# Kernel optimization log

Measured on AMD Instinct MI355X. Metric: run time of the kernel, lower is better.

## Reference

```python
import jax, jax.numpy as jnp
import numpy as np

B, S, N, DEG, KC = 4, 12, 8192, 16, 3
SEQ = S - KC + 1  # 10
H, LAYER, HID, MLP_H = 4, 3, 3, 64
NEG = -1e9


def setup_inputs() -> dict:
    key = jax.random.key(0)
    ks = jax.random.split(key, 40)
    f = lambda i, shp, sc=0.2: jax.random.normal(ks[i], shp, jnp.float32) * sc
    # deterministic unique edge list: DEG distinct neighbors per source node
    src = np.repeat(np.arange(N), DEG)
    dst = (src + 1 + np.tile(np.arange(DEG), N) * 37) % N
    edges = jnp.asarray(np.stack([src, dst]).astype(np.int32))
    return dict(
        occ=jax.random.normal(ks[0], (B, S, N), jnp.float32),
        prc_l=jax.random.uniform(ks[1], (B, N), jnp.float32),
        edges=edges,
        values=jnp.ones((N * DEG,), jnp.float32),
        conv_w=f(2, (1, 1, KC, 2)), conv_b=f(3, (1,)),
        gat_W=f(4, (H, SEQ, SEQ)), gat_a=f(5, (H, 2 * SEQ)),
        gat_lin_w=f(6, (1, H)), gat_lin_b=f(7, (1,)),
        gcn_w=f(8, (SEQ, SEQ)), gcn_b=f(9, (SEQ,)),
        Wih0=f(10, (4 * HID, LAYER)), Whh0=f(11, (4 * HID, HID)), bih0=f(12, (4 * HID,)), bhh0=f(13, (4 * HID,)),
        Wih1=f(14, (4 * HID, HID)), Whh1=f(15, (4 * HID, HID)), bih1=f(16, (4 * HID,)), bhh1=f(17, (4 * HID,)),
        Qw=f(18, (SEQ, SEQ)), Kw=f(19, (SEQ, SEQ)), Vw=f(20, (SEQ, SEQ)),
        m1w1=f(21, (MLP_H, SEQ)), m1b1=f(22, (MLP_H,)),
        m1w2=f(23, (MLP_H // 2, MLP_H)), m1b2=f(24, (MLP_H // 2,)),
        m1w3=f(25, (1, MLP_H // 2)), m1b3=f(26, (1,)),
        m2w1=f(27, (8 * (LAYER + 1), LAYER + 1)), m2b1=f(28, (8 * (LAYER + 1),)),
        m2w2=f(29, (4 * (LAYER + 1), 8 * (LAYER + 1))), m2b2=f(30, (4 * (LAYER + 1),)),
        m2w3=f(31, (1, 4 * (LAYER + 1))), m2b3=f(32, (1,)),
    )


def _lstm_layer(x, Wih, Whh, bih, bhh):
    # x: [T, Bn, in] time-major; PyTorch gate order i,f,g,o
    Bn, hdim = x.shape[1], Whh.shape[1]
    def step(carry, xt):
        h, c = carry
        g = xt @ Wih.T + h @ Whh.T + bih + bhh
        i, fg, gg, o = jnp.split(g, 4, axis=1)
        c = jax.nn.sigmoid(fg) * c + jax.nn.sigmoid(i) * jnp.tanh(gg)
        h = jax.nn.sigmoid(o) * jnp.tanh(c)
        return (h, c), h
    init = (jnp.zeros((Bn, hdim), x.dtype), jnp.zeros((Bn, hdim), x.dtype))
    _, hs = jax.lax.scan(step, init, x)
    return hs  # [T, Bn, hdim]


def _gat(x2, src, dst, values, mask, gat_W, gat_a, lin_w, lin_b):
    # x2: [b*n, seq]; only first N rows are gathered (faithful to the original)
    h = jnp.einsum('ns,hso->hno', x2, gat_W)                 # [H, b*n, seq]
    eh = jnp.concatenate([h[:, src, :], h[:, dst, :]], 2)    # [H, E, 2*seq]
    atts = jax.nn.leaky_relu(jnp.einsum('hed,hd->he', eh, gat_a), 0.2)  # [H, E]
    mt = atts.T @ lin_w.T + lin_b                            # [E, 1]
    new_vals = values * mt[:, 0]
    n = mask.shape[0]
    dense = jnp.zeros((n, n), x2.dtype).at[src, dst].add(new_vals)
    return jax.nn.softmax(dense + mask, axis=0)              # softmax over dim 0, as nn.Softmax(dim=0)


def reference(occ, prc_l, edges, values, conv_w, conv_b, gat_W, gat_a, gat_lin_w, gat_lin_b, gcn_w, gcn_b, Wih0, Whh0, bih0, bhh0, Wih1, Whh1, bih1, bhh1, Qw, Kw, Vw, m1w1, m1b1, m1w2, m1b2, m1w3, m1b3, m2w1, m2b1, m2w2, m2b2, m2w3, m2b3):
    b, s, n = occ.shape
    seq = s - conv_w.shape[2] + 1
    occ_t = jnp.transpose(occ, (0, 2, 1))                    # [b, n, s]
    prc = jnp.broadcast_to(prc_l[:, :, None], (b, n, s))
    fea = jnp.stack([occ_t, prc], axis=3).reshape(b * n, s, 2)[:, None]  # [bn,1,s,2]
    fea = jax.lax.conv_general_dilated(fea, conv_w, (1, 1), 'VALID',
                                       dimension_numbers=('NCHW', 'OIHW', 'NCHW'))
    fea = (fea + conv_b[None, :, None, None]).reshape(b, n, seq)
    src, dst = edges[0], edges[1]
    mask = jnp.full((n, n), NEG, occ.dtype).at[src, dst].set(0.0)
    lrelu = lambda z: jax.nn.leaky_relu(z, 0.01)
    gcn = lambda z: lrelu(z @ gcn_w.T + gcn_b)
    A1 = _gat(fea.reshape(b * n, seq), src, dst, values, mask, gat_W, gat_a, gat_lin_w, gat_lin_b)
    c1 = gcn(jnp.einsum('nm,bms->bns', A1, fea))
    A2 = _gat(c1.reshape(b * n, seq), src, dst, values, mask, gat_W, gat_a, gat_lin_w, gat_lin_b)
    c2 = gcn(jnp.einsum('nm,bms->bns', A2, c1))
    xt = jnp.stack([fea, c1, c2], axis=3).reshape(b * n, seq, 3)
    xT = jnp.transpose(xt, (1, 0, 2))                        # time-major [seq, bn, 3]
    h0 = _lstm_layer(xT, Wih0, Whh0, bih0, bhh0)
    h1 = _lstm_layer(h0, Wih1, Whh1, bih1, bhh1)
    x_long = jnp.transpose(h1, (1, 0, 2))                    # [bn, seq, 3]
    y_long = x_long[:, -1, 0]                                # [bn]
    xl = jnp.transpose(x_long, (0, 2, 1))                    # [bn, 3, seq]
    Q = xl @ Qw.T
    K = xl @ Kw.T
    V = xl @ Vw.T
    alpha = jax.nn.softmax(jnp.einsum('bis,bjs->bij', Q, K) / jnp.float32(V.shape[1]), axis=2)
    att = jnp.einsum('bij,bjs->bis', alpha, V)               # [bn, 3, seq]
    h = jax.nn.relu(att @ m1w1.T + m1b1)
    h = jax.nn.relu(h @ m1w2.T + m1b2)
    att_out = (h @ m1w3.T + m1b3)[:, :, 0]                   # [bn, 3]
    temp = jnp.concatenate([y_long[:, None], att_out], axis=1)  # [bn, 4]
    h = jax.nn.relu(temp @ m2w1.T + m2b1)
    h = jax.nn.relu(h @ m2w2.T + m2b2)
    y = (h @ m2w3.T + m2b3)[:, 0]
    return y.reshape(b, n)
```

## Files before the change

### kernel.cpp

```cpp
#include <hip/hip_runtime.h>

#define NN    8192
#define BB    4
#define SS    12
#define SEQL  10
#define SEQP  16
#define KCC   3
#define DEGN  16
#define EE    (NN*DEGN)
#define HHH   4
#define HIDN  3
#define BN    (BB*NN)

__device__ __forceinline__ float fexp(float x)  { return __expf(x); }
__device__ __forceinline__ float fsig(float x)  { return __fdividef(1.0f, 1.0f + __expf(-x)); }

__global__ __launch_bounds__(256) void k_fea_node(const float* __restrict__ occ,
                                                  const float* __restrict__ prc,
                                                  const float* __restrict__ convw,
                                                  const float* __restrict__ convb,
                                                  const float* __restrict__ gatW,
                                                  const float* __restrict__ gata,
                                                  float* __restrict__ fea,
                                                  float* __restrict__ p1p2) {
    int t = blockIdx.x * blockDim.x + threadIdx.x;
    if (t >= BN) return;
    int b = t >> 13, nn = t & (NN - 1);
    float o[SS];
    const float* op = occ + (size_t)b * SS * NN + nn;
#pragma unroll
    for (int s = 0; s < SS; s++) o[s] = op[(size_t)s * NN];
    float w0[KCC], w1s = 0.f;
#pragma unroll
    for (int k = 0; k < KCC; k++) { w0[k] = convw[k * 2]; w1s += convw[k * 2 + 1]; }
    float base = prc[t] * w1s + convb[0];
    float fv[SEQL];
#pragma unroll
    for (int tt = 0; tt < SEQL; tt++) {
        float acc = base;
#pragma unroll
        for (int k = 0; k < KCC; k++) acc += o[tt + k] * w0[k];
        fv[tt] = acc;
    }
    float* f = fea + (size_t)t * SEQP;
    *(float4*)(f)     = make_float4(fv[0], fv[1], fv[2], fv[3]);
    *(float4*)(f + 4) = make_float4(fv[4], fv[5], fv[6], fv[7]);
    *(float2*)(f + 8) = make_float2(fv[8], fv[9]);
    if (t < NN) {
#pragma unroll
        for (int hh = 0; hh < HHH; hh++) {
            float p1 = 0.f, p2 = 0.f;
#pragma unroll
            for (int oo = 0; oo < SEQL; oo++) {
                float hv = 0.f;
#pragma unroll
                for (int s = 0; s < SEQL; s++) hv += fv[s] * gatW[hh * (SEQL * SEQL) + s * SEQL + oo];
                p1 += hv * gata[hh * (2 * SEQL) + oo];
                p2 += hv * gata[hh * (2 * SEQL) + SEQL + oo];
            }
            p1p2[t * 8 + hh]     = p1;
            p1p2[t * 8 + 4 + hh] = p2;
        }
    }
}

__global__ __launch_bounds__(256) void k_colmt(const float* __restrict__ values,
                                               const float* __restrict__ p1p2,
                                               const float* __restrict__ linw,
                                               const float* __restrict__ linb,
                                               float* __restrict__ mt,
                                               float2* __restrict__ colms) {
    int u = blockIdx.x * blockDim.x + threadIdx.x;
    int q = u & 3, j = u >> 2;
    float p2l[HHH], lw[HHH];
#pragma unroll
    for (int hh = 0; hh < HHH; hh++) { p2l[hh] = p1p2[j * 8 + 4 + hh]; lw[hh] = linw[hh]; }
    float lb = linb[0];
    float v[4];
#pragma unroll
    for (int dd = 0; dd < 4; dd++) {
        int d = q * 4 + dd;
        int s = (j - 1 - d * 37) & (NN - 1);
        int e = s * DEGN + d;
        float4 p1v = *(const float4*)(p1p2 + s * 8);
        float a0 = p1v.x + p2l[0]; a0 = a0 > 0.f ? a0 : 0.2f * a0;
        float a1 = p1v.y + p2l[1]; a1 = a1 > 0.f ? a1 : 0.2f * a1;
        float a2 = p1v.z + p2l[2]; a2 = a2 > 0.f ? a2 : 0.2f * a2;
        float a3 = p1v.w + p2l[3]; a3 = a3 > 0.f ? a3 : 0.2f * a3;
        float acc = lb + a0*lw[0] + a1*lw[1] + a2*lw[2] + a3*lw[3];
        float m_ = acc * values[e];
        v[dd] = m_;
        mt[e] = m_;
    }
    float m = fmaxf(fmaxf(v[0], v[1]), fmaxf(v[2], v[3]));
    m = fmaxf(m, __shfl_xor(m, 1));
    m = fmaxf(m, __shfl_xor(m, 2));
    float sum = 0.f;
#pragma unroll
    for (int dd = 0; dd < 4; dd++) sum += fexp(v[dd] - m);
    sum += __shfl_xor(sum, 1);
    sum += __shfl_xor(sum, 2);
    if (q == 0) colms[j] = make_float2(m, __fdividef(1.0f, sum));
}

template <int DOP>
__global__ __launch_bounds__(256) void k_agg(const int* __restrict__ edges,
                                             const float* __restrict__ mt,
                                             const float2* __restrict__ colms,
                                             const float* __restrict__ xin,
                                             const float* __restrict__ gcnw,
                                             const float* __restrict__ gcnb,
                                             const float* __restrict__ gatW,
                                             const float* __restrict__ gata,
                                             float* __restrict__ xout,
                                             float* __restrict__ p1p2) {
    int u = blockIdx.x * blockDim.x + threadIdx.x;
    int q = u & 7, t = u >> 3;
    int b = t >> 13, i = t & (NN - 1);
    int e0 = i * DEGN + q * 2;
    int2   dn2 = *(const int2*)(edges + EE + e0);
    float2 mt2 = *(const float2*)(mt + e0);
    int dns[2] = {dn2.x, dn2.y};
    float mts[2] = {mt2.x, mt2.y};
    float acc[SEQL];
#pragma unroll
    for (int s = 0; s < SEQL; s++) acc[s] = 0.f;
#pragma unroll
    for (int dd = 0; dd < 2; dd++) {
        int dn = dns[dd];
        float2 ms = colms[dn];
        float w = fexp(mts[dd] - ms.x) * ms.y;
        const float* xr = xin + ((size_t)b * NN + dn) * SEQP;
        float4 v0 = *(const float4*)(xr);
        float4 v1 = *(const float4*)(xr + 4);
        float2 v2 = *(const float2*)(xr + 8);
        acc[0] += w*v0.x; acc[1] += w*v0.y; acc[2] += w*v0.z; acc[3] += w*v0.w;
        acc[4] += w*v1.x; acc[5] += w*v1.y; acc[6] += w*v1.z; acc[7] += w*v1.w;
        acc[8] += w*v2.x; acc[9] += w*v2.y;
    }
#pragma unroll
    for (int s = 0; s < SEQL; s++) acc[s] += __shfl_xor(acc[s], 1);
#pragma unroll
    for (int s = 0; s < SEQL; s++) acc[s] += __shfl_xor(acc[s], 2);
#pragma unroll
    for (int s = 0; s < SEQL; s++) acc[s] += __shfl_xor(acc[s], 4);

    float co[SEQL];
#pragma unroll
    for (int o = 0; o < SEQL; o++) {
        float a = gcnb[o];
#pragma unroll
        for (int s = 0; s < SEQL; s++) a += acc[s] * gcnw[o * SEQL + s];
        co[o] = a > 0.f ? a : 0.01f * a;
    }
    if (q == 0) {
        float* xo = xout + (size_t)t * SEQP;
        *(float4*)(xo)     = make_float4(co[0], co[1], co[2], co[3]);
        *(float4*)(xo + 4) = make_float4(co[4], co[5], co[6], co[7]);
        *(float2*)(xo + 8) = make_float2(co[8], co[9]);
    }
    if (DOP && t < NN && q < 4) {
        float hv[SEQL];
#pragma unroll
        for (int oo = 0; oo < SEQL; oo++) hv[oo] = 0.f;
#pragma unroll
        for (int s = 0; s < SEQL; s++) {
            const float2* wr = (const float2*)(gatW + q * (SEQL*SEQL) + s * SEQL);
#pragma unroll
            for (int p = 0; p < 5; p++) {
                float2 wv = wr[p];
                hv[2*p]   += co[s] * wv.x;
                hv[2*p+1] += co[s] * wv.y;
            }
        }
        const float2* ga1 = (const float2*)(gata + q * (2*SEQL));
        const float2* ga2 = (const float2*)(gata + q * (2*SEQL) + SEQL);
        float p1 = 0.f, p2 = 0.f;
#pragma unroll
        for (int p = 0; p < 5; p++) {
            float2 a1 = ga1[p], a2 = ga2[p];
            p1 += hv[2*p] * a1.x + hv[2*p+1] * a1.y;
            p2 += hv[2*p] * a2.x + hv[2*p+1] * a2.y;
        }
        p1p2[t * 8 + q]     = p1;
        p1p2[t * 8 + 4 + q] = p2;
    }
}

__global__ __launch_bounds__(256) void k_lstm_att(
    const float* __restrict__ fea, const float* __restrict__ c1g, const float* __restrict__ c2g,
    const float* __restrict__ Wih0, const float* __restrict__ Whh0,
    const float* __restrict__ bih0, const float* __restrict__ bhh0,
    const float* __restrict__ Wih1, const float* __restrict__ Whh1,
    const float* __restrict__ bih1, const float* __restrict__ bhh1,
    const float* __restrict__ Qw, const float* __restrict__ Kw, const float* __restrict__ Vw,
    float* __restrict__ attrow) {

    int u = blockIdx.x * blockDim.x + threadIdx.x;
    int e = u & 1;
    int t = u >> 1;

    float fr[SEQL], c1r[SEQL], c2r[SEQL];
    {
        const float* a = fea + (size_t)t * SEQP;
        const float* b = c1g + (size_t)t * SEQP;
        const float* c = c2g + (size_t)t * SEQP;
        float4 a0 = *(const float4*)a, a1 = *(const float4*)(a+4); float2 a2 = *(const float2*)(a+8);
        float4 b0 = *(const float4*)b, b1 = *(const float4*)(b+4); float2 b2 = *(const float2*)(b+8);
        float4 d0 = *(const float4*)c, d1 = *(const float4*)(c+4); float2 d2 = *(const float2*)(c+8);
        fr[0]=a0.x; fr[1]=a0.y; fr[2]=a0.z; fr[3]=a0.w; fr[4]=a1.x; fr[5]=a1.y; fr[6]=a1.z; fr[7]=a1.w; fr[8]=a2.x; fr[9]=a2.y;
        c1r[0]=b0.x; c1r[1]=b0.y; c1r[2]=b0.z; c1r[3]=b0.w; c1r[4]=b1.x; c1r[5]=b1.y; c1r[6]=b1.z; c1r[7]=b1.w; c1r[8]=b2.x; c1r[9]=b2.y;
        c2r[0]=d0.x; c2r[1]=d0.y; c2r[2]=d0.z; c2r[3]=d0.w; c2r[4]=d1.x; c2r[5]=d1.y; c2r[6]=d1.z; c2r[7]=d1.w; c2r[8]=d2.x; c2r[9]=d2.y;
    }

    int r0 = e * 6;
    float W0[6][6], B0[6], W1[6][6], B1[6];
#pragma unroll
    for (int k = 0; k < 6; k++) {
        int r = r0 + k;
        W0[k][0]=Wih0[r*3]; W0[k][1]=Wih0[r*3+1]; W0[k][2]=Wih0[r*3+2];
        W0[k][3]=Whh0[r*3]; W0[k][4]=Whh0[r*3+1]; W0[k][5]=Whh0[r*3+2];
        B0[k]=bih0[r]+bhh0[r];
        W1[k][0]=Wih1[r*3]; W1[k][1]=Wih1[r*3+1]; W1[k][2]=Wih1[r*3+2];
        W1[k][3]=Whh1[r*3]; W1[k][4]=Whh1[r*3+1]; W1[k][5]=Whh1[r*3+2];
        B1[k]=bih1[r]+bhh1[r];
    }
    float two_e = e ? 2.f : 1.f;
    float neg_e = e ? -1.f : 0.f;

    float c0[3]={0,0,0}, c1s[3]={0,0,0}, h0[3]={0,0,0}, h1[3]={0,0,0};
    float hist[SEQL][HIDN];
#pragma unroll
    for (int st = 0; st < SEQL; st++) {
        float tt[6], pp[6];
        {
            float x0 = fr[st], x1 = c1r[st], x2 = c2r[st];
#pragma unroll
            for (int k = 0; k < 6; k++) {
                float g = B0[k] + x0*W0[k][0] + x1*W0[k][1] + x2*W0[k][2]
                                + h0[0]*W0[k][3] + h0[1]*W0[k][4] + h0[2]*W0[k][5];
                if (k < 3) { float uu = fsig(two_e * g); tt[k] = two_e * uu + neg_e; }
                else       { tt[k] = fsig(g); }
            }
#pragma unroll
            for (int k = 0; k < 6; k++) pp[k] = __shfl_xor(tt[k], 1);
#pragma unroll
            for (int j = 0; j < 3; j++) {
                float si = e ? pp[j]   : tt[j];
                float sf = e ? pp[3+j] : tt[3+j];
                float tg = e ? tt[j]   : pp[j];
                float so = e ? tt[3+j] : pp[3+j];
                float cn = sf * c0[j] + si * tg;
                c0[j] = cn;
                h0[j] = so * (2.f * fsig(2.f * cn) - 1.f);
            }
        }
        {
#pragma unroll
            for (int k = 0; k < 6; k++) {
                float g = B1[k] + h0[0]*W1[k][0] + h0[1]*W1[k][1] + h0[2]*W1[k][2]
                                + h1[0]*W1[k][3] + h1[1]*W1[k][4] + h1[2]*W1[k][5];
                if (k < 3) { float uu = fsig(two_e * g); tt[k] = two_e * uu + neg_e; }
                else       { tt[k] = fsig(g); }
            }
#pragma unroll
            for (int k = 0; k < 6; k++) pp[k] = __shfl_xor(tt[k], 1);
#pragma unroll
            for (int j = 0; j < 3; j++) {
                float si = e ? pp[j]   : tt[j];
                float sf = e ? pp[3+j] : tt[3+j];
                float tg = e ? tt[j]   : pp[j];
                float so = e ? tt[3+j] : pp[3+j];
                float cn = sf * c1s[j] + si * tg;
                c1s[j] = cn;
                h1[j] = so * (2.f * fsig(2.f * cn) - 1.f);
            }
        }
#pragma unroll
        for (int j = 0; j < 3; j++) hist[st][j] = h1[j];
    }

    float V[3][5];
    float sc[3][3];
#pragma unroll
    for (int a = 0; a < 3; a++)
#pragma unroll
        for (int j = 0; j < 3; j++) sc[a][j] = 0.f;
#pragma unroll
    for (int p = 0; p < 5; p++) {
        int o = 2 * p + e;
        float wq[SEQL], wk[SEQL], wv[SEQL];
        const float2* q2 = (const float2*)(Qw + o * SEQL);
        const float2* k2 = (const float2*)(Kw + o * SEQL);
        const float2* v2 = (const float2*)(Vw + o * SEQL);
#pragma unroll
        for (int z = 0; z < 5; z++) {
            float2 a = q2[z], b = k2[z], c = v2[z];
            wq[2*z] = a.x; wq[2*z+1] = a.y;
            wk[2*z] = b.x; wk[2*z+1] = b.y;
            wv[2*z] = c.x; wv[2*z+1] = c.y;
        }
        float qj[3], kj[3];
#pragma unroll
        for (int j = 0; j < 3; j++) {
            float qv = 0.f, kv = 0.f, vv = 0.f;
#pragma unroll
            for (int s = 0; s < SEQL; s++) {
                float xv = hist[s][j];
                qv += xv * wq[s]; kv += xv * wk[s]; vv += xv * wv[s];
            }
            qj[j] = qv; kj[j] = kv; V[j][p] = vv;
        }
#pragma unroll
        for (int a = 0; a < 3; a++)
#pragma unroll
            for (int j = 0; j < 3; j++) sc[a][j] += qj[a] * kj[j];
    }
#pragma unroll
    for (int a = 0; a < 3; a++)
#pragma unroll
        for (int j = 0; j < 3; j++) sc[a][j] += __shfl_xor(sc[a][j], 1);

    float* ar = attrow + (size_t)t * 32;
#pragma unroll
    for (int a = 0; a < 3; a++) {
        float s0 = sc[a][0] * (1.f/3.f), s1 = sc[a][1] * (1.f/3.f), s2 = sc[a][2] * (1.f/3.f);
        float m = fmaxf(s0, fmaxf(s1, s2));
        float e0 = fexp(s0-m), e1 = fexp(s1-m), e2 = fexp(s2-m);
        float inv = __fdividef(1.0f, e0 + e1 + e2);
#pragma unroll
        for (int p = 0; p < 5; p++)
            ar[a * SEQL + 2*p + e] = (e0*V[0][p] + e1*V[1][p] + e2*V[2][p]) * inv;
    }
    if (e == 0) ar[30] = hist[SEQL-1][0];
}

__global__ __launch_bounds__(256, 2) void k_head(
    const float* __restrict__ attrow,
    const float* __restrict__ m1w1, const float* __restrict__ m1b1,
    const float* __restrict__ m1w2, const float* __restrict__ m1b2,
    const float* __restrict__ m1w3, const float* __restrict__ m1b3,
    const float* __restrict__ m2w1, const float* __restrict__ m2b1,
    const float* __restrict__ m2w2, const float* __restrict__ m2b2,
    const float* __restrict__ m2w3, const float* __restrict__ m2b3,
    float* __restrict__ out) {

    __shared__ float lw[3717];
    int tid = threadIdx.x;
    for (int z = tid; z < 1024; z += 256) {
        int qq = z >> 8, kk = (z >> 4) & 15, s = z & 15;
        if (s < 12) lw[qq*200 + kk*12 + s] = (s < 10) ? m1w1[(qq*16+kk)*10 + s] : 0.f;
    }
    for (int z = tid; z < 2048; z += 256) {
        int qq = z >> 9, rem = z & 511, r = rem >> 4, kk = rem & 15;
        lw[800 + qq*520 + r*16 + kk] = m1w2[r*64 + qq*16 + kk];
    }
    for (int z = tid; z < 64;  z += 256) lw[2880 + z] = m1b1[z];
    for (int z = tid; z < 32;  z += 256) { lw[2944 + z] = m1b2[z]; lw[2976 + z] = m1w3[z]; }
    for (int z = tid; z < 128; z += 256) lw[3012 + z] = m2w1[z];
    for (int z = tid; z < 32;  z += 256) lw[3140 + z] = m2b1[z];
    for (int z = tid; z < 512; z += 256) lw[3172 + z] = m2w2[z];
    for (int z = tid; z < 16;  z += 256) { lw[3684 + z] = m2b2[z]; lw[3700 + z] = m2w3[z]; }
    if (tid == 0) { lw[3008] = m1b3[0]; lw[3716] = m2b3[0]; }
    __syncthreads();

    int u = blockIdx.x * blockDim.x + tid;
    int q = u & 3;
    int t = u >> 2;

    const float* w1b = lw + q * 200;
    float hb0[16], hb1[16], hb2a[16];
    float ylong;
    {
        float row[32];
        const float4* arp = (const float4*)(attrow + (size_t)t * 32);
#pragma unroll
        for (int p = 0; p < 8; p++) {
            float4 z = arp[p];
            row[4*p] = z.x; row[4*p+1] = z.y; row[4*p+2] = z.z; row[4*p+3] = z.w;
        }
        ylong = row[30];
#pragma unroll 4
        for (int kk = 0; kk < 16; kk++) {
            float4 wa = *(const float4*)(w1b + kk*12);
            float4 wb = *(const float4*)(w1b + kk*12 + 4);
            float4 wc = *(const float4*)(w1b + kk*12 + 8);
            float bk = lw[2880 + q*16 + kk];
            float a0 = bk
                + row[0]*wa.x + row[1]*wa.y + row[2]*wa.z + row[3]*wa.w
                + row[4]*wb.x + row[5]*wb.y + row[6]*wb.z + row[7]*wb.w
                + row[8]*wc.x + row[9]*wc.y;
            float a1 = bk
                + row[10]*wa.x + row[11]*wa.y + row[12]*wa.z + row[13]*wa.w
                + row[14]*wb.x + row[15]*wb.y + row[16]*wb.z + row[17]*wb.w
                + row[18]*wc.x + row[19]*wc.y;
            float a2 = bk
                + row[20]*wa.x + row[21]*wa.y + row[22]*wa.z + row[23]*wa.w
                + row[24]*wb.x + row[25]*wb.y + row[26]*wb.z + row[27]*wb.w
                + row[28]*wc.x + row[29]*wc.y;
            hb0[kk] = a0 > 0.f ? a0 : 0.f;
            hb1[kk] = a1 > 0.f ? a1 : 0.f;
            hb2a[kk] = a2 > 0.f ? a2 : 0.f;
        }
    }

    const float* w2b = lw + 800 + q * 520;
    float ao0 = lw[3008], ao1 = ao0, ao2 = ao0;
#pragma unroll 4
    for (int r = 0; r < 32; r++) {
        const float4* wr = (const float4*)(w2b + r * 16);
        float4 w0 = wr[0], w1 = wr[1], w2 = wr[2], w3 = wr[3];
        float p0 = hb0[0]*w0.x + hb0[1]*w0.y + hb0[2]*w0.z + hb0[3]*w0.w
                 + hb0[4]*w1.x + hb0[5]*w1.y + hb0[6]*w1.z + hb0[7]*w1.w
                 + hb0[8]*w2.x + hb0[9]*w2.y + hb0[10]*w2.z + hb0[11]*w2.w
                 + hb0[12]*w3.x + hb0[13]*w3.y + hb0[14]*w3.z + hb0[15]*w3.w;
        float p1 = hb1[0]*w0.x + hb1[1]*w0.y + hb1[2]*w0.z + hb1[3]*w0.w
                 + hb1[4]*w1.x + hb1[5]*w1.y + hb1[6]*w1.z + hb1[7]*w1.w
                 + hb1[8]*w2.x + hb1[9]*w2.y + hb1[10]*w2.z + hb1[11]*w2.w
                 + hb1[12]*w3.x + hb1[13]*w3.y + hb1[14]*w3.z + hb1[15]*w3.w;
        float p2 = hb2a[0]*w0.x + hb2a[1]*w0.y + hb2a[2]*w0.z + hb2a[3]*w0.w
                 + hb2a[4]*w1.x + hb2a[5]*w1.y + hb2a[6]*w1.z + hb2a[7]*w1.w
                 + hb2a[8]*w2.x + hb2a[9]*w2.y + hb2a[10]*w2.z + hb2a[11]*w2.w
                 + hb2a[12]*w3.x + hb2a[13]*w3.y + hb2a[14]*w3.z + hb2a[15]*w3.w;
        p0 += __shfl_xor(p0, 1); p0 += __shfl_xor(p0, 2);
        p1 += __shfl_xor(p1, 1); p1 += __shfl_xor(p1, 2);
        p2 += __shfl_xor(p2, 1); p2 += __shfl_xor(p2, 2);
        float bb = lw[2944 + r], ww = lw[2976 + r];
        float t0 = p0 + bb; t0 = t0 > 0.f ? t0 : 0.f;
        float t1 = p1 + bb; t1 = t1 > 0.f ? t1 : 0.f;
        float t2 = p2 + bb; t2 = t2 > 0.f ? t2 : 0.f;
        ao0 += t0 * ww; ao1 += t1 * ww; ao2 += t2 * ww;
    }

    float hb2[32];
#pragma unroll 8
    for (int k = 0; k < 32; k++) {
        float4 wv = *(const float4*)(lw + 3012 + k*4);
        float a = lw[3140 + k] + ylong*wv.x + ao0*wv.y + ao1*wv.z + ao2*wv.w;
        hb2[k] = a > 0.f ? a : 0.f;
    }
    float y = lw[3716];
#pragma unroll 4
    for (int r = 0; r < 16; r++) {
        float a = lw[3684 + r];
        const float4* wr = (const float4*)(lw + 3172 + r*32);
#pragma unroll
        for (int c = 0; c < 8; c++) {
            float4 wv = wr[c];
            a += hb2[4*c]*wv.x + hb2[4*c+1]*wv.y + hb2[4*c+2]*wv.z + hb2[4*c+3]*wv.w;
        }
        float h = a > 0.f ? a : 0.f;
        y += h * lw[3700 + r];
    }
    if (q == 0) out[t] = y;
}

extern "C" void kernel_launch(void* const* d_in, const int* in_sizes, int n_in,
                              void* d_out, int out_size, void* d_ws, size_t ws_size,
                              hipStream_t stream) {
    const float* occ    = (const float*)d_in[0];
    const float* prc    = (const float*)d_in[1];
    const int*   edges  = (const int*)  d_in[2];
    const float* values = (const float*)d_in[3];
    const float* convw  = (const float*)d_in[4];
    const float* convb  = (const float*)d_in[5];
    const float* gatW   = (const float*)d_in[6];
    const float* gata   = (const float*)d_in[7];
    const float* linw   = (const float*)d_in[8];
    const float* linb   = (const float*)d_in[9];
    const float* gcnw   = (const float*)d_in[10];
    const float* gcnb   = (const float*)d_in[11];
    const float* Wih0   = (const float*)d_in[12];
    const float* Whh0   = (const float*)d_in[13];
    const float* bih0   = (const float*)d_in[14];
    const float* bhh0   = (const float*)d_in[15];
    const float* Wih1   = (const float*)d_in[16];
    const float* Whh1   = (const float*)d_in[17];
    const float* bih1   = (const float*)d_in[18];
    const float* bhh1   = (const float*)d_in[19];
    const float* Qw     = (const float*)d_in[20];
    const float* Kw     = (const float*)d_in[21];
    const float* Vw     = (const float*)d_in[22];
    const float* m1w1   = (const float*)d_in[23];
    const float* m1b1   = (const float*)d_in[24];
    const float* m1w2   = (const float*)d_in[25];
    const float* m1b2   = (const float*)d_in[26];
    const float* m1w3   = (const float*)d_in[27];
    const float* m1b3   = (const float*)d_in[28];
    const float* m2w1   = (const float*)d_in[29];
    const float* m2b1   = (const float*)d_in[30];
    const float* m2w2   = (const float*)d_in[31];
    const float* m2b2   = (const float*)d_in[32];
    const float* m2w3   = (const float*)d_in[33];
    const float* m2b3   = (const float*)d_in[34];
    float* out = (float*)d_out;

    char* ws = (char*)d_ws;
    float*  fea    = (float*) (ws);
    float*  c1     = (float*) (ws + 2097152);
    float*  c2     = (float*) (ws + 4194304);
    float*  p1p2   = (float*) (ws + 6291456);
    float*  mt     = (float*) (ws + 6553600);
    float2* colms  = (float2*)(ws + 7077888);
    float*  attrow = (float*) (ws + 7143424);

    k_fea_node<<<128, 256, 0, stream>>>(occ, prc, convw, convb, gatW, gata, fea, p1p2);

    k_colmt<<<128, 256, 0, stream>>>(values, p1p2, linw, linb, mt, colms);
    k_agg<1><<<1024, 256, 0, stream>>>(edges, mt, colms, fea, gcnw, gcnb,
                                       gatW, gata, c1, p1p2);

    k_colmt<<<128, 256, 0, stream>>>(values, p1p2, linw, linb, mt, colms);
    k_agg<0><<<1024, 256, 0, stream>>>(edges, mt, colms, c1, gcnw, gcnb,
                                       gatW, gata, c2, p1p2);

    k_lstm_att<<<256, 256, 0, stream>>>(fea, c1, c2,
        Wih0, Whh0, bih0, bhh0, Wih1, Whh1, bih1, bhh1, Qw, Kw, Vw, attrow);

    k_head<<<512, 256, 0, stream>>>(attrow,
        m1w1, m1b1, m1w2, m1b2, m1w3, m1b3,
        m2w1, m2b1, m2w2, m2b2, m2w3, m2b3, out);
}
```

Before: 78.22 us.

## Fuse LSTM-attention kernel with MLP head kernel

Merges the LSTM/attention kernel and the MLP head kernel into one launch. Attention outputs are exchanged via warp shuffles and kept in registers instead of being written to and reread from a global attrow buffer. Each node now uses four threads, so the LSTM/attention computation is duplicated across thread pairs, and the combined kernel carries higher register pressure.

```diff
diff --git a/kernel.cpp b/kernel.cpp
--- a/kernel.cpp
+++ b/kernel.cpp
@@ -187,18 +187,44 @@
     }
 }
 
-__global__ __launch_bounds__(256) void k_lstm_att(
+__global__ __launch_bounds__(256, 2) void k_lstm_head(
     const float* __restrict__ fea, const float* __restrict__ c1g, const float* __restrict__ c2g,
     const float* __restrict__ Wih0, const float* __restrict__ Whh0,
     const float* __restrict__ bih0, const float* __restrict__ bhh0,
     const float* __restrict__ Wih1, const float* __restrict__ Whh1,
     const float* __restrict__ bih1, const float* __restrict__ bhh1,
     const float* __restrict__ Qw, const float* __restrict__ Kw, const float* __restrict__ Vw,
-    float* __restrict__ attrow) {
-
-    int u = blockIdx.x * blockDim.x + threadIdx.x;
-    int e = u & 1;
-    int t = u >> 1;
+    const float* __restrict__ m1w1, const float* __restrict__ m1b1,
+    const float* __restrict__ m1w2, const float* __restrict__ m1b2,
+    const float* __restrict__ m1w3, const float* __restrict__ m1b3,
+    const float* __restrict__ m2w1, const float* __restrict__ m2b1,
+    const float* __restrict__ m2w2, const float* __restrict__ m2b2,
+    const float* __restrict__ m2w3, const float* __restrict__ m2b3,
+    float* __restrict__ out) {
+
+    __shared__ float lw[3717];
+    int tid = threadIdx.x;
+    for (int z = tid; z < 1024; z += 256) {
+        int qq = z >> 8, kk = (z >> 4) & 15, s = z & 15;
+        if (s < 12) lw[qq*200 + kk*12 + s] = (s < 10) ? m1w1[(qq*16+kk)*10 + s] : 0.f;
+    }
+    for (int z = tid; z < 2048; z += 256) {
+        int qq = z >> 9, rem = z & 511, r = rem >> 4, kk = rem & 15;
+        lw[800 + qq*520 + r*16 + kk] = m1w2[r*64 + qq*16 + kk];
+    }
+    for (int z = tid; z < 64;  z += 256) lw[2880 + z] = m1b1[z];
+    for (int z = tid; z < 32;  z += 256) { lw[2944 + z] = m1b2[z]; lw[2976 + z] = m1w3[z]; }
+    for (int z = tid; z < 128; z += 256) lw[3012 + z] = m2w1[z];
+    for (int z = tid; z < 32;  z += 256) lw[3140 + z] = m2b1[z];
+    for (int z = tid; z < 512; z += 256) lw[3172 + z] = m2w2[z];
+    for (int z = tid; z < 16;  z += 256) { lw[3684 + z] = m2b2[z]; lw[3700 + z] = m2w3[z]; }
+    if (tid == 0) { lw[3008] = m1b3[0]; lw[3716] = m2b3[0]; }
+    __syncthreads();
+
+    int u = blockIdx.x * blockDim.x + tid;
+    int q = u & 3;
+    int t = u >> 2;
+    int e = q & 1;
 
     float fr[SEQL], c1r[SEQL], c2r[SEQL];
     {
@@ -321,7 +347,7 @@
 #pragma unroll
         for (int j = 0; j < 3; j++) sc[a][j] += __shfl_xor(sc[a][j], 1);
 
-    float* ar = attrow + (size_t)t * 32;
+    float row[32];
 #pragma unroll
     for (int a = 0; a < 3; a++) {
         float s0 = sc[a][0] * (1.f/3.f), s1 = sc[a][1] * (1.f/3.f), s2 = sc[a][2] * (1.f/3.f);
@@ -329,79 +355,39 @@
         float e0 = fexp(s0-m), e1 = fexp(s1-m), e2 = fexp(s2-m);
         float inv = __fdividef(1.0f, e0 + e1 + e2);
 #pragma unroll
-        for (int p = 0; p < 5; p++)
-            ar[a * SEQL + 2*p + e] = (e0*V[0][p] + e1*V[1][p] + e2*V[2][p]) * inv;
-    }
-    if (e == 0) ar[30] = hist[SEQL-1][0];
-}
-
-__global__ __launch_bounds__(256, 2) void k_head(
-    const float* __restrict__ attrow,
-    const float* __restrict__ m1w1, const float* __restrict__ m1b1,
-    const float* __restrict__ m1w2, const float* __restrict__ m1b2,
-    const float* __restrict__ m1w3, const float* __restrict__ m1b3,
-    const float* __restrict__ m2w1, const float* __restrict__ m2b1,
-    const float* __restrict__ m2w2, const float* __restrict__ m2b2,
-    const float* __restrict__ m2w3, const float* __restrict__ m2b3,
-    float* __restrict__ out) {
-
-    __shared__ float lw[3717];
-    int tid = threadIdx.x;
-    for (int z = tid; z < 1024; z += 256) {
-        int qq = z >> 8, kk = (z >> 4) & 15, s = z & 15;
-        if (s < 12) lw[qq*200 + kk*12 + s] = (s < 10) ? m1w1[(qq*16+kk)*10 + s] : 0.f;
-    }
-    for (int z = tid; z < 2048; z += 256) {
-        int qq = z >> 9, rem = z & 511, r = rem >> 4, kk = rem & 15;
-        lw[800 + qq*520 + r*16 + kk] = m1w2[r*64 + qq*16 + kk];
-    }
-    for (int z = tid; z < 64;  z += 256) lw[2880 + z] = m1b1[z];
-    for (int z = tid; z < 32;  z += 256) { lw[2944 + z] = m1b2[z]; lw[2976 + z] = m1w3[z]; }
-    for (int z = tid; z < 128; z += 256) lw[3012 + z] = m2w1[z];
-    for (int z = tid; z < 32;  z += 256) lw[3140 + z] = m2b1[z];
-    for (int z = tid; z < 512; z += 256) lw[3172 + z] = m2w2[z];
-    for (int z = tid; z < 16;  z += 256) { lw[3684 + z] = m2b2[z]; lw[3700 + z] = m2w3[z]; }
-    if (tid == 0) { lw[3008] = m1b3[0]; lw[3716] = m2b3[0]; }
-    __syncthreads();
-
-    int u = blockIdx.x * blockDim.x + tid;
-    int q = u & 3;
-    int t = u >> 2;
+        for (int p = 0; p < 5; p++) {
+            float av = (e0*V[0][p] + e1*V[1][p] + e2*V[2][p]) * inv;
+            float pv = __shfl_xor(av, 1);
+            row[a * SEQL + 2*p + e]       = av;
+            row[a * SEQL + 2*p + (1 - e)] = pv;
+        }
+    }
+    float ylong = hist[SEQL-1][0];
+    row[30] = ylong; row[31] = 0.f;
 
     const float* w1b = lw + q * 200;
     float hb0[16], hb1[16], hb2a[16];
-    float ylong;
-    {
-        float row[32];
-        const float4* arp = (const float4*)(attrow + (size_t)t * 32);
-#pragma unroll
-        for (int p = 0; p < 8; p++) {
-            float4 z = arp[p];
-            row[4*p] = z.x; row[4*p+1] = z.y; row[4*p+2] = z.z; row[4*p+3] = z.w;
-        }
-        ylong = row[30];
 #pragma unroll 4
-        for (int kk = 0; kk < 16; kk++) {
-            float4 wa = *(const float4*)(w1b + kk*12);
-            float4 wb = *(const float4*)(w1b + kk*12 + 4);
-            float4 wc = *(const float4*)(w1b + kk*12 + 8);
-            float bk = lw[2880 + q*16 + kk];
-            float a0 = bk
-                + row[0]*wa.x + row[1]*wa.y + row[2]*wa.z + row[3]*wa.w
-                + row[4]*wb.x + row[5]*wb.y + row[6]*wb.z + row[7]*wb.w
-                + row[8]*wc.x + row[9]*wc.y;
-            float a1 = bk
-                + row[10]*wa.x + row[11]*wa.y + row[12]*wa.z + row[13]*wa.w
-                + row[14]*wb.x + row[15]*wb.y + row[16]*wb.z + row[17]*wb.w
-                + row[18]*wc.x + row[19]*wc.y;
-            float a2 = bk
-                + row[20]*wa.x + row[21]*wa.y + row[22]*wa.z + row[23]*wa.w
-                + row[24]*wb.x + row[25]*wb.y + row[26]*wb.z + row[27]*wb.w
-                + row[28]*wc.x + row[29]*wc.y;
-            hb0[kk] = a0 > 0.f ? a0 : 0.f;
-            hb1[kk] = a1 > 0.f ? a1 : 0.f;
-            hb2a[kk] = a2 > 0.f ? a2 : 0.f;
-        }
+    for (int kk = 0; kk < 16; kk++) {
+        float4 wa = *(const float4*)(w1b + kk*12);
+        float4 wb = *(const float4*)(w1b + kk*12 + 4);
+        float4 wc = *(const float4*)(w1b + kk*12 + 8);
+        float bk = lw[2880 + q*16 + kk];
+        float a0 = bk
+            + row[0]*wa.x + row[1]*wa.y + row[2]*wa.z + row[3]*wa.w
+            + row[4]*wb.x + row[5]*wb.y + row[6]*wb.z + row[7]*wb.w
+            + row[8]*wc.x + row[9]*wc.y;
+        float a1 = bk
+            + row[10]*wa.x + row[11]*wa.y + row[12]*wa.z + row[13]*wa.w
+            + row[14]*wb.x + row[15]*wb.y + row[16]*wb.z + row[17]*wb.w
+            + row[18]*wc.x + row[19]*wc.y;
+        float a2 = bk
+            + row[20]*wa.x + row[21]*wa.y + row[22]*wa.z + row[23]*wa.w
+            + row[24]*wb.x + row[25]*wb.y + row[26]*wb.z + row[27]*wb.w
+            + row[28]*wc.x + row[29]*wc.y;
+        hb0[kk] = a0 > 0.f ? a0 : 0.f;
+        hb1[kk] = a1 > 0.f ? a1 : 0.f;
+        hb2a[kk] = a2 > 0.f ? a2 : 0.f;
     }
 
     const float* w2b = lw + 800 + q * 520;
@@ -502,7 +488,6 @@
     float*  p1p2   = (float*) (ws + 6291456);
     float*  mt     = (float*) (ws + 6553600);
     float2* colms  = (float2*)(ws + 7077888);
-    float*  attrow = (float*) (ws + 7143424);
 
     k_fea_node<<<128, 256, 0, stream>>>(occ, prc, convw, convb, gatW, gata, fea, p1p2);
 
@@ -514,10 +499,8 @@
     k_agg<0><<<1024, 256, 0, stream>>>(edges, mt, colms, c1, gcnw, gcnb,
                                        gatW, gata, c2, p1p2);
 
-    k_lstm_att<<<256, 256, 0, stream>>>(fea, c1, c2,
-        Wih0, Whh0, bih0, bhh0, Wih1, Whh1, bih1, bhh1, Qw, Kw, Vw, attrow);
-
-    k_head<<<512, 256, 0, stream>>>(attrow,
+    k_lstm_head<<<512, 256, 0, stream>>>(fea, c1, c2,
+        Wih0, Whh0, bih0, bhh0, Wih1, Whh1, bih1, bhh1, Qw, Kw, Vw,
         m1w1, m1b1, m1w2, m1b2, m1w3, m1b3,
         m2w1, m2b1, m2w2, m2b2, m2w3, m2b3, out);
 }
```

Result: slower. 87.97 us (+12.5%).
